# Kernel optimization log

Hardware: AMD Instinct MI355X
Metric: run time of the kernel (lower is better)

The kernel has to match this reference:

```python
import jax, jax.numpy as jnp
import numpy as np

N, NEMB, NHID = 8192, 256, 64
NEG_INF = jnp.float32(-9e15)


def setup_inputs() -> dict:
    key = jax.random.key(0)
    k_x, k_adj, k_w, k_a1, k_a2 = jax.random.split(key, 5)
    x = jax.random.normal(k_x, (N, NEMB), dtype=jnp.float32)
    adj = jax.random.randint(k_adj, (N, N), 0, 2, dtype=jnp.int32)
    # xavier-ish scales
    Ww = jax.random.normal(k_w, (NEMB, NHID), dtype=jnp.float32) * (1.0 / np.sqrt(NEMB + NHID))
    Wb = jnp.zeros((NHID,), dtype=jnp.float32)
    a1 = jax.random.normal(k_a1, (NHID,), dtype=jnp.float32) * (1.0 / np.sqrt(2 * NHID + 1))
    a2 = jax.random.normal(k_a2, (NHID,), dtype=jnp.float32) * (1.0 / np.sqrt(2 * NHID + 1))
    ab = jnp.zeros((1,), dtype=jnp.float32)
    return {"x": x, "adj": adj, "Ww": Ww, "Wb": Wb, "a1": a1, "a2": a2, "ab": ab}


def reference(x, adj, Ww, Wb, a1, a2, ab):
    # h = self.w(x)
    h = x @ Ww + Wb  # [N, nhid]
    # Pairwise score e[i,j] = leaky_relu(a . [h_i, h_j] + b), computed WITHOUT
    # materializing the [N*N, 2*nhid] concat tensor (same math, decomposed linear).
    f_src = h @ a1  # [N] contribution of h_i (first half of concat)
    f_dst = h @ a2  # [N] contribution of h_j (second half of concat)
    e = jax.nn.leaky_relu(f_src[:, None] + f_dst[None, :] + ab[0], negative_slope=0.01)  # [N, N]
    # Faithful masked_scatter_ semantics: True positions (row-major) receive
    # e.flatten() elements taken sequentially (compacted), not positionally.
    mflat = (adj > 0).reshape(-1)
    pos = jnp.clip(jnp.cumsum(mflat.astype(jnp.int32)) - 1, 0)
    vals = e.reshape(-1)[pos]
    att = jnp.where(mflat, vals, NEG_INF).reshape(e.shape)
    att = jax.nn.softmax(att, axis=1)
    # dropout disabled (dropout=0)
    out = jax.nn.elu(att @ h)  # [N, nhid]
    return out
```

## Files before the change

### kernel.cpp

```cpp
#include <hip/hip_runtime.h>
#include <hip/hip_bf16.h>

#define N 8192
#define NEMB 256
#define NHID 64
#define LOG2E 1.4426950408889634f

typedef __attribute__((ext_vector_type(8))) short short8;
typedef __attribute__((ext_vector_type(4))) float f32x4;

__device__ __forceinline__ float elu_f(float x) {
    return x > 0.f ? x : __expf(x) - 1.f;
}

__device__ __forceinline__ float exp2_fast(float x) {
#if __has_builtin(__builtin_amdgcn_exp2f)
    return __builtin_amdgcn_exp2f(x);
#else
    return exp2f(x);
#endif
}

__device__ __forceinline__ short f2bf(float f) {
    union { float f; unsigned u; } c; c.f = f;
    unsigned r = c.u + 0x7fffu + ((c.u >> 16) & 1u);
    return (short)(r >> 16);
}

__device__ __forceinline__ float bf2f(short s) {
    union { unsigned u; float f; } c; c.u = ((unsigned)(unsigned short)s) << 16;
    return c.f;
}

__global__ __launch_bounds__(256) void k01_prologue(
    const int* __restrict__ adj, unsigned long long* __restrict__ bits,
    unsigned int* __restrict__ cnt,
    const float* __restrict__ x, const float* __restrict__ Ww,
    const float* __restrict__ Wb, const float* __restrict__ a1,
    const float* __restrict__ a2, short* __restrict__ hT,
    float* __restrict__ fs, float* __restrict__ fd)
{
    int t = threadIdx.x;
    if (blockIdx.x < N) {
        int row = blockIdx.x;
        int lane = t & 63;
        const int* arow = adj + (size_t)row * N;
        unsigned long long* brow = bits + (size_t)row * (N / 64);
        __shared__ unsigned int wcs[16];
        unsigned int c = 0;
        for (int it = 0; it < 8; it++) {
            int j = it * 1024 + t * 4;
            int4 a = *(const int4*)&arow[j];
            unsigned int nb = (unsigned)(a.x > 0) | ((unsigned)(a.y > 0) << 1) |
                              ((unsigned)(a.z > 0) << 2) | ((unsigned)(a.w > 0) << 3);
            unsigned int v8  = nb  | (__shfl_down((int)nb, 1, 64) << 4);
            unsigned int v16 = v8  | (__shfl_down((int)v8, 2, 64) << 8);
            unsigned int v32 = v16 | (__shfl_down((int)v16, 4, 64) << 16);
            unsigned int hi  = (unsigned int)__shfl_down((int)v32, 8, 64);
            if ((lane & 15) == 0) {
                unsigned long long word = (unsigned long long)v32 |
                                          ((unsigned long long)hi << 32);
                brow[it * 16 + (t >> 4)] = word;
                c += __popcll(word);
            }
        }
        if ((t & 15) == 0) wcs[t >> 4] = c;
        __syncthreads();
        if (t == 0) {
            unsigned int s = 0;
            for (int i = 0; i < 16; i++) s += wcs[i];
            cnt[row] = s;
        }
    } else {
        __shared__ float xs[4 * NEMB];
        int rowblk = (blockIdx.x - N) * 4;
        for (int i = 0; i < 4; i++)
            xs[i * NEMB + t] = x[(size_t)rowblk * NEMB + i * NEMB + t];
        __syncthreads();
        int rl = t >> 6;
        int k  = t & 63;
        float acc = Wb[k];
        const float* xrow = &xs[rl * NEMB];
#pragma unroll 8
        for (int c = 0; c < NEMB; c++)
            acc = fmaf(xrow[c], Ww[c * NHID + k], acc);
        int row = rowblk + rl;
        hT[(size_t)k * N + row] = f2bf(acc);
        float s1 = acc * a1[k];
        float s2 = acc * a2[k];
        for (int o = 32; o > 0; o >>= 1) {
            s1 += __shfl_down(s1, o, 64);
            s2 += __shfl_down(s2, o, 64);
        }
        if (k == 0) { fs[row] = s1; fd[row] = s2; }
    }
}

#define SEGW 16

__global__ __launch_bounds__(512, 4) void k4_mfma(
    const unsigned long long* __restrict__ bits,
    const unsigned int* __restrict__ cnt,
    const float* __restrict__ fs, const float* __restrict__ fd,
    const float* __restrict__ ab, const short* __restrict__ hT,
    float* __restrict__ out)
{
    __shared__ float fdl[N];
    __shared__ float dred[8 * 1024];
    __shared__ float fsl[32];
    __shared__ float rsum[8 * 16];
    __shared__ unsigned int red512[512];
    __shared__ unsigned int rb16[16];

    int t = threadIdx.x;
    int bid = blockIdx.x;
    int wv = t >> 6;
    int L = t & 63;
    int m = L & 15;
    int g = L >> 4;
    int m0 = bid * 16;
    int row = m0 + m;
    float ab0 = ab[0];

    for (int i = 0; i < 4; ++i) {
        int fi = i * 2048 + t * 4;
        float4 v4 = *(const float4*)&fd[fi];
        v4.x *= LOG2E; v4.y *= LOG2E; v4.z *= LOG2E; v4.w *= LOG2E;
        *(float4*)&fdl[fi] = v4;
    }
    unsigned int c16 = 0;
    if (t < bid) {
        const uint4* cp = (const uint4*)(cnt + t * 16);
        uint4 q0 = cp[0], q1 = cp[1], q2 = cp[2], q3 = cp[3];
        c16 = q0.x + q0.y + q0.z + q0.w + q1.x + q1.y + q1.z + q1.w +
              q2.x + q2.y + q2.z + q2.w + q3.x + q3.y + q3.z + q3.w;
    }
    red512[t] = c16;
    __syncthreads();
#pragma unroll
    for (int o = 256; o > 0; o >>= 1) {
        if (t < o) red512[t] += red512[t + o];
        __syncthreads();
    }
    unsigned int rowbase0 = red512[0];
    if (t == 0) {
        unsigned int s = rowbase0;
#pragma unroll
        for (int i = 0; i < 16; ++i) { rb16[i] = s; s += cnt[m0 + i]; }
    }
    unsigned int fs0 = rowbase0 >> 13;
    if (t < 32) {
        unsigned int idx = fs0 + (unsigned)t;
        if (idx > 8191u) idx = 8191u;
        fsl[t] = (fs[idx] + ab0) * LOG2E;
    }
    __syncthreads();

    unsigned int rbm = rb16[m];
    unsigned int w13 = rbm >> 13;
    float s0 = fsl[w13 - fs0];
    unsigned int i1 = w13 + 1 - fs0; if (i1 > 31u) i1 = 31u;
    float s1 = fsl[i1];
    unsigned int Rstar = (w13 + 1u) << 13;

    const unsigned long long* brow = bits + (size_t)row * (N / 64);
    int w0 = wv * SEGW;
    unsigned int part = 0;
    for (int w = g; w < w0; w += 4) part += (unsigned)__popcll(brow[w]);
    part += __shfl_xor(part, 16, 64);
    part += __shfl_xor(part, 32, 64);
    unsigned int base = rbm + part;

    f32x4 acc0 = {0.f,0.f,0.f,0.f}, acc1 = {0.f,0.f,0.f,0.f};
    f32x4 acc2 = {0.f,0.f,0.f,0.f}, acc3 = {0.f,0.f,0.f,0.f};
    float psum = 0.f;
    const short* hpm = hT + (size_t)m * N;

    for (int w = w0; w < w0 + SEGW; ++w) {
        unsigned long long w64 = brow[w];
#pragma unroll
        for (int hh = 0; hh < 2; ++hh) {
            int off = hh * 32 + g * 8;
            unsigned int n = (unsigned)__popcll(w64 & ((1ull << off) - 1ull));
            unsigned int u = (unsigned int)(w64 >> off) & 0xffu;
            unsigned int pu[8];
#pragma unroll
            for (int j = 0; j < 8; ++j) {
                unsigned int bit = (u >> j) & 1u;
                unsigned int r = base + n;
                float d = fdl[r & 8191u];
                float sv = (r >= Rstar) ? s1 : s0;
                float v = sv + d;
                float lr = fmaxf(v, 0.01f * v);
                float p = exp2_fast(lr);
                p = bit ? p : 0.f;
                psum += p;
                union { float f; unsigned u; } cv; cv.f = p;
                pu[j] = cv.u + 0x8000u;
                n += bit;
            }
            union { short8 v; unsigned q[4]; } afu;
#pragma unroll
            for (int k = 0; k < 4; ++k)
                afu.q[k] = __builtin_amdgcn_perm(pu[2 * k + 1], pu[2 * k],
                                                 0x07060302u);
            const short* hp = hpm + w * 64 + off;
            short8 b0 = *(const short8*)(hp);
            short8 b1 = *(const short8*)(hp + 16 * N);
            short8 b2 = *(const short8*)(hp + 32 * N);
            short8 b3 = *(const short8*)(hp + 48 * N);
            acc0 = __builtin_amdgcn_mfma_f32_16x16x32_bf16(afu.v, b0, acc0, 0, 0, 0);
            acc1 = __builtin_amdgcn_mfma_f32_16x16x32_bf16(afu.v, b1, acc1, 0, 0, 0);
            acc2 = __builtin_amdgcn_mfma_f32_16x16x32_bf16(afu.v, b2, acc2, 0, 0, 0);
            acc3 = __builtin_amdgcn_mfma_f32_16x16x32_bf16(afu.v, b3, acc3, 0, 0, 0);
        }
        base += (unsigned)__popcll(w64);
    }

    psum += __shfl_xor(psum, 16, 64);
    psum += __shfl_xor(psum, 32, 64);
    if (L < 16) rsum[wv * 16 + m] = psum;
    float* dw = &dred[wv * 1024];
#pragma unroll
    for (int reg = 0; reg < 4; ++reg) {
        int lrow = g * 4 + reg;
        dw[lrow * 64 + m     ] = acc0[reg];
        dw[lrow * 64 + m + 16] = acc1[reg];
        dw[lrow * 64 + m + 32] = acc2[reg];
        dw[lrow * 64 + m + 48] = acc3[reg];
    }
    __syncthreads();

#pragma unroll
    for (int q = 0; q < 2; ++q) {
        int o = q * 512 + t;
        int lrow = o >> 6, col = o & 63;
        float s = 0.f;
#pragma unroll
        for (int v8 = 0; v8 < 8; ++v8) s += dred[v8 * 1024 + o];
        float rs = 0.f;
#pragma unroll
        for (int v8 = 0; v8 < 8; ++v8) rs += rsum[v8 * 16 + lrow];
        int grow = m0 + lrow;
        float res;
        if (cnt[grow] == 0u) {
            float hs = 0.f;
            const short* hp = hT + (size_t)col * N;
            for (int j = 0; j < N; ++j) hs += bf2f(hp[j]);
            res = hs * (1.0f / 8192.0f);
        } else {
            res = s / rs;
        }
        out[(size_t)grow * NHID + col] = elu_f(res);
    }
}

extern "C" void kernel_launch(void* const* d_in, const int* in_sizes, int n_in,
                              void* d_out, int out_size, void* d_ws, size_t ws_size,
                              hipStream_t stream)
{
    const float* x   = (const float*)d_in[0];
    const int*   adj = (const int*)d_in[1];
    const float* Ww  = (const float*)d_in[2];
    const float* Wb  = (const float*)d_in[3];
    const float* a1  = (const float*)d_in[4];
    const float* a2  = (const float*)d_in[5];
    const float* ab  = (const float*)d_in[6];
    float* out = (float*)d_out;

    char* ws = (char*)d_ws;
    float* fs = (float*)(ws + 0);
    float* fd = (float*)(ws + 32768);
    unsigned int* cnt = (unsigned int*)(ws + 65536);
    short* hT = (short*)(ws + 98304);
    unsigned long long* bits = (unsigned long long*)(ws + 98304 + 1048576);

    k01_prologue<<<N + N / 4, 256, 0, stream>>>(adj, bits, cnt,
                                                x, Ww, Wb, a1, a2, hT, fs, fd);
    k4_mfma<<<N / 16, 512, 0, stream>>>(bits, cnt, fs, fd, ab, hT, out);
}
```

Baseline: 465.3 us.

## Compute softmax row sums via MFMA with ones and shrink reduction LDS

Several changes. The row-sum of probabilities is now an extra MFMA against a vector of bf16 ones, which removes the per-element scalar adds and the shuffle reductions. The bf16 packing uses the hardware v_cvt_pk_bf16_f32 instruction in place of manual rounding plus perm. The cross-wave accumulator reduction uses half the LDS (4 slabs, with a two-phase add), which may raise occupancy. The x staging load is vectorised with float4, and the prefix popcount loop now loads two words per iteration. The extra MFMA adds matrix work, and the row sum now comes from bf16-rounded values, which slightly changes the numerics.

After: 458.7 us. Within noise of the previous version (-1.4%).

```diff
diff --git a/kernel.cpp b/kernel.cpp
--- a/kernel.cpp
+++ b/kernel.cpp
@@ -74,8 +74,7 @@
     } else {
         __shared__ float xs[4 * NEMB];
         int rowblk = (blockIdx.x - N) * 4;
-        for (int i = 0; i < 4; i++)
-            xs[i * NEMB + t] = x[(size_t)rowblk * NEMB + i * NEMB + t];
+        *(float4*)&xs[t * 4] = *(const float4*)&x[(size_t)rowblk * NEMB + t * 4];
         __syncthreads();
         int rl = t >> 6;
         int k  = t & 63;
@@ -106,7 +105,7 @@
     float* __restrict__ out)
 {
     __shared__ float fdl[N];
-    __shared__ float dred[8 * 1024];
+    __shared__ float dred[4 * 1024];
     __shared__ float fsl[32];
     __shared__ float rsum[8 * 16];
     __shared__ unsigned int red512[512];
@@ -166,14 +165,22 @@
     const unsigned long long* brow = bits + (size_t)row * (N / 64);
     int w0 = wv * SEGW;
     unsigned int part = 0;
-    for (int w = g; w < w0; w += 4) part += (unsigned)__popcll(brow[w]);
+    for (int w = g * 2; w < w0; w += 8) {
+        unsigned long long pb0 = brow[w];
+        unsigned long long pb1 = brow[w + 1];
+        part += (unsigned)__popcll(pb0) + (unsigned)__popcll(pb1);
+    }
     part += __shfl_xor(part, 16, 64);
     part += __shfl_xor(part, 32, 64);
     unsigned int base = rbm + part;
 
+    short8 ones8;
+#pragma unroll
+    for (int k = 0; k < 8; ++k) ones8[k] = (short)0x3f80;
+
     f32x4 acc0 = {0.f,0.f,0.f,0.f}, acc1 = {0.f,0.f,0.f,0.f};
     f32x4 acc2 = {0.f,0.f,0.f,0.f}, acc3 = {0.f,0.f,0.f,0.f};
-    float psum = 0.f;
+    f32x4 acc4 = {0.f,0.f,0.f,0.f};
     const short* hpm = hT + (size_t)m * N;
 
     for (int w = w0; w < w0 + SEGW; ++w) {
@@ -183,7 +190,7 @@
             int off = hh * 32 + g * 8;
             unsigned int n = (unsigned)__popcll(w64 & ((1ull << off) - 1ull));
             unsigned int u = (unsigned int)(w64 >> off) & 0xffu;
-            unsigned int pu[8];
+            float pf[8];
 #pragma unroll
             for (int j = 0; j < 8; ++j) {
                 unsigned int bit = (u >> j) & 1u;
@@ -193,17 +200,17 @@
                 float v = sv + d;
                 float lr = fmaxf(v, 0.01f * v);
                 float p = exp2_fast(lr);
-                p = bit ? p : 0.f;
-                psum += p;
-                union { float f; unsigned u; } cv; cv.f = p;
-                pu[j] = cv.u + 0x8000u;
+                pf[j] = bit ? p : 0.f;
                 n += bit;
             }
             union { short8 v; unsigned q[4]; } afu;
 #pragma unroll
-            for (int k = 0; k < 4; ++k)
-                afu.q[k] = __builtin_amdgcn_perm(pu[2 * k + 1], pu[2 * k],
-                                                 0x07060302u);
+            for (int k = 0; k < 4; ++k) {
+                unsigned qk;
+                asm("v_cvt_pk_bf16_f32 %0, %1, %2"
+                    : "=v"(qk) : "v"(pf[2 * k]), "v"(pf[2 * k + 1]));
+                afu.q[k] = qk;
+            }
             const short* hp = hpm + w * 64 + off;
             short8 b0 = *(const short8*)(hp);
             short8 b1 = *(const short8*)(hp + 16 * N);
@@ -213,31 +220,48 @@
             acc1 = __builtin_amdgcn_mfma_f32_16x16x32_bf16(afu.v, b1, acc1, 0, 0, 0);
             acc2 = __builtin_amdgcn_mfma_f32_16x16x32_bf16(afu.v, b2, acc2, 0, 0, 0);
             acc3 = __builtin_amdgcn_mfma_f32_16x16x32_bf16(afu.v, b3, acc3, 0, 0, 0);
+            acc4 = __builtin_amdgcn_mfma_f32_16x16x32_bf16(afu.v, ones8, acc4, 0, 0, 0);
         }
         base += (unsigned)__popcll(w64);
     }
 
-    psum += __shfl_xor(psum, 16, 64);
-    psum += __shfl_xor(psum, 32, 64);
-    if (L < 16) rsum[wv * 16 + m] = psum;
-    float* dw = &dred[wv * 1024];
-#pragma unroll
-    for (int reg = 0; reg < 4; ++reg) {
-        int lrow = g * 4 + reg;
-        dw[lrow * 64 + m     ] = acc0[reg];
-        dw[lrow * 64 + m + 16] = acc1[reg];
-        dw[lrow * 64 + m + 32] = acc2[reg];
-        dw[lrow * 64 + m + 48] = acc3[reg];
+    if (m == 0) {
+#pragma unroll
+        for (int reg = 0; reg < 4; ++reg)
+            rsum[wv * 16 + g * 4 + reg] = acc4[reg];
+    }
+
+    float* dw = &dred[(wv & 3) * 1024];
+    if (wv < 4) {
+#pragma unroll
+        for (int reg = 0; reg < 4; ++reg) {
+            int lrow = g * 4 + reg;
+            dw[lrow * 64 + m     ] = acc0[reg];
+            dw[lrow * 64 + m + 16] = acc1[reg];
+            dw[lrow * 64 + m + 32] = acc2[reg];
+            dw[lrow * 64 + m + 48] = acc3[reg];
+        }
     }
     __syncthreads();
-
-#pragma unroll
-    for (int q = 0; q < 2; ++q) {
-        int o = q * 512 + t;
+    if (wv >= 4) {
+#pragma unroll
+        for (int reg = 0; reg < 4; ++reg) {
+            int lrow = g * 4 + reg;
+            dw[lrow * 64 + m     ] += acc0[reg];
+            dw[lrow * 64 + m + 16] += acc1[reg];
+            dw[lrow * 64 + m + 32] += acc2[reg];
+            dw[lrow * 64 + m + 48] += acc3[reg];
+        }
+    }
+    __syncthreads();
+
+#pragma unroll
+    for (int qq = 0; qq < 2; ++qq) {
+        int o = qq * 512 + t;
         int lrow = o >> 6, col = o & 63;
         float s = 0.f;
 #pragma unroll
-        for (int v8 = 0; v8 < 8; ++v8) s += dred[v8 * 1024 + o];
+        for (int v4 = 0; v4 < 4; ++v4) s += dred[v4 * 1024 + o];
         float rs = 0.f;
 #pragma unroll
         for (int v8 = 0; v8 < 8; ++v8) rs += rsum[v8 * 16 + lrow];
```
